# Kernel tuning notes

Measured on AMD Instinct MI355X. Metric: run time of the kernel, lower is better.

Reference implementation:

```python
import jax, jax.numpy as jnp
import numpy as np

NUM_HEAD = 16
HIDDEN = 1024
HEAD_DIM = HIDDEN // NUM_HEAD


def setup_inputs() -> dict:
    key = jax.random.key(0)
    k1, k2, k3, k4, k5 = jax.random.split(key, 5)
    scale = 0.02
    x = jax.random.normal(k1, (2, 2048, HIDDEN), dtype=jnp.float32)
    w_in = jax.random.normal(k2, (3 * HIDDEN, HIDDEN), dtype=jnp.float32) * scale
    b_in = jax.random.normal(k3, (3 * HIDDEN,), dtype=jnp.float32) * scale
    w_out = jax.random.normal(k4, (HIDDEN, HIDDEN), dtype=jnp.float32) * scale
    b_out = jax.random.normal(k5, (HIDDEN,), dtype=jnp.float32) * scale
    return {"x": x, "w_in": w_in, "b_in": b_in, "w_out": w_out, "b_out": b_out}


def reference(x, w_in, b_in, w_out, b_out):
    B, S, D = x.shape
    # in_proj: fused QKV, torch Linear convention y = x @ W.T + b
    qkv = x @ w_in.T + b_in                      # [B,S,3D]
    q, k, v = jnp.split(qkv, 3, axis=-1)         # each [B,S,D]
    def heads(t):
        return t.reshape(B, S, NUM_HEAD, HEAD_DIM).transpose(0, 2, 1, 3)  # [B,H,S,d]
    q, k, v = heads(q), heads(k), heads(v)
    scores = jnp.einsum("bhqd,bhkd->bhqk", q, k) / jnp.sqrt(
        jnp.asarray(HEAD_DIM, dtype=x.dtype))    # [B,H,S,S]
    attn = jax.nn.softmax(scores, axis=-1)
    out = jnp.einsum("bhqk,bhkd->bhqd", attn, v)  # [B,H,S,d]
    out = out.transpose(0, 2, 1, 3).reshape(B, S, D)
    return out @ w_out.T + b_out
```

## Files before the change

### kernel.cpp

```cpp
#include <hip/hip_runtime.h>

using u16 = unsigned short;
using u32 = unsigned int;

typedef __bf16 bf16x8 __attribute__((ext_vector_type(8)));
typedef __bf16 bf16x2 __attribute__((ext_vector_type(2)));
typedef float f32x4 __attribute__((ext_vector_type(4)));

__device__ __forceinline__ u16 f2b(float x) {
  u32 u = __builtin_bit_cast(u32, x);
  u += 0x7fffu + ((u >> 16) & 1u);
  return (u16)(u >> 16);
}

__device__ __forceinline__ u32 pk2(float lo, float hi) {
  bf16x2 t;
  t[0] = (__bf16)lo;
  t[1] = (__bf16)hi;
  return __builtin_bit_cast(u32, t);
}

__device__ __forceinline__ void gload16(const u16* g, u16* l) {
  __builtin_amdgcn_global_load_lds(
      (const __attribute__((address_space(1))) void*)g,
      (__attribute__((address_space(3))) void*)l, 16, 0, 0);
}

#define SCALE_Q 0.1803368801111204f
#define DEFER_THR 8.0f

__global__ void cvt_bf16_k(const float* __restrict__ s, u16* __restrict__ d, int n8) {
  int i = blockIdx.x * blockDim.x + threadIdx.x;
  int stride = gridDim.x * blockDim.x;
  for (; i < n8; i += stride) {
    float4 a = ((const float4*)s)[2 * i];
    float4 b = ((const float4*)s)[2 * i + 1];
    uint4 o;
    o.x = (u32)f2b(a.x) | ((u32)f2b(a.y) << 16);
    o.y = (u32)f2b(a.z) | ((u32)f2b(a.w) << 16);
    o.z = (u32)f2b(b.x) | ((u32)f2b(b.y) << 16);
    o.w = (u32)f2b(b.z) | ((u32)f2b(b.w) << 16);
    ((uint4*)d)[i] = o;
  }
}

template <int MODE, int BM>
__global__ __launch_bounds__(256) void gemm_bt(
    const u16* __restrict__ A, const u16* __restrict__ Bm,
    const float* __restrict__ bias,
    u16* __restrict__ q, u16* __restrict__ k, u16* __restrict__ v,
    float* __restrict__ outf) {
  constexpr int KD = 1024;
  constexpr int MR = BM / 32;
  constexpr int CA = BM / 8;
  const int n0 = blockIdx.x * 128;
  const int m0 = blockIdx.y * BM;
  const int tid = threadIdx.x;
  const int wid = tid >> 6;
  const int lane = tid & 63;
  const int wr = wid >> 1, wc = wid & 1;
  const int fr = lane & 15, fg = lane >> 4;
  const int srow = lane >> 3;
  const int scol = ((lane & 7) ^ (srow & 7)) * 8;

  __shared__ __align__(16) u16 As[BM * 64];
  __shared__ __align__(16) u16 Bs[128 * 64];

  f32x4 acc[MR][4] = {};

  for (int k0 = 0; k0 < KD; k0 += 64) {
#pragma unroll
    for (int i = 0; i < CA / 4; ++i) {
      const int chunk = wid * (CA / 4) + i;
      gload16(A + (size_t)(m0 + chunk * 8 + srow) * KD + k0 + scol, As + chunk * 512);
    }
#pragma unroll
    for (int i = 0; i < 4; ++i) {
      const int chunk = wid * 4 + i;
      gload16(Bm + (size_t)(n0 + chunk * 8 + srow) * KD + k0 + scol, Bs + chunk * 512);
    }
    __syncthreads();
#pragma unroll
    for (int ks = 0; ks < 2; ++ks) {
      bf16x8 af[MR], bfr[4];
#pragma unroll
      for (int r = 0; r < MR; ++r) {
        const int row = wr * (BM / 2) + r * 16 + fr;
        af[r] = *(const bf16x8*)(As + row * 64 + ((ks * 32 + fg * 8) ^ ((row & 7) * 8)));
      }
#pragma unroll
      for (int c = 0; c < 4; ++c) {
        const int row = wc * 64 + c * 16 + fr;
        bfr[c] = *(const bf16x8*)(Bs + row * 64 + ((ks * 32 + fg * 8) ^ ((row & 7) * 8)));
      }
#pragma unroll
      for (int r = 0; r < MR; ++r)
#pragma unroll
        for (int c = 0; c < 4; ++c)
          acc[r][c] = __builtin_amdgcn_mfma_f32_16x16x32_bf16(af[r], bfr[c], acc[r][c], 0, 0, 0);
    }
    __syncthreads();
  }

#pragma unroll
  for (int r = 0; r < MR; ++r) {
#pragma unroll
    for (int c = 0; c < 4; ++c) {
      const int gcol = n0 + wc * 64 + c * 16 + fr;
      const float bv = bias[gcol];
#pragma unroll
      for (int g = 0; g < 4; ++g) {
        const int grow = m0 + wr * (BM / 2) + r * 16 + fg * 4 + g;
        float val = acc[r][c][g] + bv;
        if (MODE == 0) {
          const int which = gcol >> 10;
          const int dcol = gcol & 1023;
          const int hh = dcol >> 6, dd = dcol & 63;
          const int bb = grow >> 11, ss = grow & 2047;
          const int bhk = (bb << 4) + hh;
          const int t = ss >> 6, sl = ss & 63;
          if (which == 0) {
            q[((size_t)bhk * 2048 + ss) * 64 + dd] = f2b(val * SCALE_Q);
          } else if (which == 1) {
            const int r_ = (sl & 32) | (((sl >> 2) & 1) << 4) | (((sl >> 4) & 1) << 3) |
                           (((sl >> 3) & 1) << 2) | (sl & 3);
            k[((size_t)bhk * 32 + t) * 4096 + r_ * 64 + (dd ^ ((r_ & 7) << 3))] = f2b(val);
          } else {
            v[((size_t)bhk * 32 + t) * 4096 + dd * 64 + (sl ^ ((dd & 7) << 3))] = f2b(val);
          }
        } else {
          outf[(size_t)grow * 1024 + gcol] = val;
        }
      }
    }
  }
}

__global__ __launch_bounds__(256) void attn_fwd(
    const u16* __restrict__ Q, const u16* __restrict__ KG,
    const u16* __restrict__ VG, u16* __restrict__ AO) {
  const int wg = blockIdx.x;
  const int newid = (wg & 7) * 64 + (wg >> 3);
  const int bh = newid >> 4;
  const int qt = newid & 15;
  const int b = bh >> 4, h = bh & 15;

  const int tid = threadIdx.x, wid = tid >> 6, lane = tid & 63;
  const int fr = lane & 15, fg = lane >> 4;
  const int q0 = qt * 128 + wid * 32;

  __shared__ __align__(16) u16 Ks[2][4096];
  __shared__ __align__(16) u16 Vs[2][4096];

  const size_t qbase = (size_t)bh * (2048 * 64);
  bf16x8 qf[2][2];
#pragma unroll
  for (int rf = 0; rf < 2; ++rf)
#pragma unroll
    for (int ks = 0; ks < 2; ++ks)
      qf[rf][ks] = *(const bf16x8*)(Q + qbase + (size_t)(q0 + rf * 16 + fr) * 64 + ks * 32 + fg * 8);

  f32x4 o[2][4] = {};
  float mrow[2] = {-3.0e38f, -3.0e38f};
  float lrow[2] = {0.f, 0.f};

  const u16* kg = KG + (size_t)bh * 131072 + tid * 8;
  const u16* vg = VG + (size_t)bh * 131072 + tid * 8;

#define STAGE(t, bufi) do {                                        \
    const u16* ksrc = kg + (t) * 4096;                             \
    const u16* vsrc = vg + (t) * 4096;                             \
    u16* kdst = (u16*)Ks[bufi] + wid * 512;                        \
    u16* vdst = (u16*)Vs[bufi] + wid * 512;                        \
    gload16(ksrc, kdst); gload16(ksrc + 2048, kdst + 2048);        \
    gload16(vsrc, vdst); gload16(vsrc + 2048, vdst + 2048);        \
  } while (0)

  STAGE(0, 0);
  __syncthreads();

  for (int t = 0; t < 32; ++t) {
    const int cur = t & 1;
    if (t + 1 < 32) STAGE(t + 1, cur ^ 1);
    const u16* kb = (const u16*)Ks[cur];
    const u16* vb = (const u16*)Vs[cur];

    bf16x8 kf[4][2], vf[4][2];
#pragma unroll
    for (int c = 0; c < 4; ++c)
#pragma unroll
      for (int ks = 0; ks < 2; ++ks)
        kf[c][ks] = *(const bf16x8*)(kb + (c * 16 + fr) * 64 + ((ks * 32 + fg * 8) ^ ((fr & 7) * 8)));
#pragma unroll
    for (int d = 0; d < 4; ++d)
#pragma unroll
      for (int ks = 0; ks < 2; ++ks)
        vf[d][ks] = *(const bf16x8*)(vb + (d * 16 + fr) * 64 + ((ks * 32 + fg * 8) ^ ((fr & 7) * 8)));

#pragma unroll
    for (int rf = 0; rf < 2; ++rf) {
      f32x4 p[4];
      __builtin_amdgcn_s_setprio(1);
#pragma unroll
      for (int c = 0; c < 4; ++c) {
        f32x4 z = {};
        z = __builtin_amdgcn_mfma_f32_16x16x32_bf16(kf[c][0], qf[rf][0], z, 0, 0, 0);
        z = __builtin_amdgcn_mfma_f32_16x16x32_bf16(kf[c][1], qf[rf][1], z, 0, 0, 0);
        p[c] = z;
      }
      __builtin_amdgcn_s_setprio(0);
      f32x4 m01 = __builtin_elementwise_max(p[0], p[1]);
      f32x4 m23 = __builtin_elementwise_max(p[2], p[3]);
      f32x4 m4 = __builtin_elementwise_max(m01, m23);
      float mx = fmaxf(fmaxf(m4[0], m4[1]), fmaxf(m4[2], m4[3]));
      mx = fmaxf(mx, __shfl_xor(mx, 16));
      mx = fmaxf(mx, __shfl_xor(mx, 32));

      const float mold = mrow[rf];
      const bool defer = __all(mx <= mold + DEFER_THR);
      float mnew = mold;
      if (!defer) {
        mnew = fmaxf(mold, mx);
        const float corr = __builtin_amdgcn_exp2f(mold - mnew);
        mrow[rf] = mnew;
        lrow[rf] *= corr;
#pragma unroll
        for (int d = 0; d < 4; ++d) o[rf][d] *= corr;
      }
#pragma unroll
      for (int c = 0; c < 4; ++c)
#pragma unroll
        for (int g = 0; g < 4; ++g)
          p[c][g] = __builtin_amdgcn_exp2f(p[c][g] - mnew);
      f32x4 s4 = (p[0] + p[1]) + (p[2] + p[3]);
      float rs = (s4[0] + s4[1]) + (s4[2] + s4[3]);
      rs += __shfl_xor(rs, 16);
      rs += __shfl_xor(rs, 32);
      lrow[rf] += rs;

      bf16x8 pa[2];
#pragma unroll
      for (int ks = 0; ks < 2; ++ks) {
        u32 w0 = pk2(p[2 * ks][0], p[2 * ks][1]);
        u32 w1 = pk2(p[2 * ks][2], p[2 * ks][3]);
        u32 w2 = pk2(p[2 * ks + 1][0], p[2 * ks + 1][1]);
        u32 w3 = pk2(p[2 * ks + 1][2], p[2 * ks + 1][3]);
        uint4 packed = {w0, w1, w2, w3};
        pa[ks] = __builtin_bit_cast(bf16x8, packed);
      }
      __builtin_amdgcn_s_setprio(1);
#pragma unroll
      for (int d = 0; d < 4; ++d) {
        o[rf][d] = __builtin_amdgcn_mfma_f32_16x16x32_bf16(vf[d][0], pa[0], o[rf][d], 0, 0, 0);
        o[rf][d] = __builtin_amdgcn_mfma_f32_16x16x32_bf16(vf[d][1], pa[1], o[rf][d], 0, 0, 0);
      }
      __builtin_amdgcn_s_setprio(0);
    }
    __syncthreads();
  }

#pragma unroll
  for (int rf = 0; rf < 2; ++rf) {
    const float rinv = __builtin_amdgcn_rcpf(lrow[rf]);
    const size_t rowoff = (size_t)(b * 2048 + q0 + rf * 16 + fr) * 1024 + h * 64;
#pragma unroll
    for (int d = 0; d < 4; ++d) {
      uint2 st;
      st.x = pk2(o[rf][d][0] * rinv, o[rf][d][1] * rinv);
      st.y = pk2(o[rf][d][2] * rinv, o[rf][d][3] * rinv);
      *(uint2*)(AO + rowoff + d * 16 + fg * 4) = st;
    }
  }
#undef STAGE
}

extern "C" void kernel_launch(void* const* d_in, const int* in_sizes, int n_in,
                              void* d_out, int out_size, void* d_ws, size_t ws_size,
                              hipStream_t stream) {
  (void)in_sizes; (void)n_in; (void)out_size; (void)ws_size;
  const float* x     = (const float*)d_in[0];
  const float* w_in  = (const float*)d_in[1];
  const float* b_in  = (const float*)d_in[2];
  const float* w_out = (const float*)d_in[3];
  const float* b_out = (const float*)d_in[4];

  u16* xb    = (u16*)d_ws;
  u16* winb  = xb    + (size_t)4096 * 1024;
  u16* woutb = winb  + (size_t)3072 * 1024;
  u16* qb    = woutb + (size_t)1024 * 1024;
  u16* kb    = qb    + (size_t)4194304;
  u16* vb    = kb    + (size_t)4194304;
  u16* aob   = vb    + (size_t)4194304;

  cvt_bf16_k<<<2048, 256, 0, stream>>>(x, xb, 4096 * 1024 / 8);
  cvt_bf16_k<<<1536, 256, 0, stream>>>(w_in, winb, 3072 * 1024 / 8);
  cvt_bf16_k<<<512, 256, 0, stream>>>(w_out, woutb, 1024 * 1024 / 8);

  gemm_bt<0, 128><<<dim3(24, 32), 256, 0, stream>>>(xb, winb, b_in, qb, kb, vb, nullptr);
  attn_fwd<<<512, 256, 0, stream>>>(qb, kb, vb, aob);
  gemm_bt<1, 64><<<dim3(8, 64), 256, 0, stream>>>(aob, woutb, b_out, nullptr, nullptr, nullptr,
                                                  (float*)d_out);
}
```

Baseline: 214.0 us.

## Merge conversions, vectorize V epilogue, prefetch two tiles, MFMA row sums

The three fp32-to-bf16 conversion launches become one kernel. The QKV GEMM epilogue now writes V as packed 8-byte stores instead of scalar stores. The attention kernel prefetches two K/V tiles ahead, using explicit vmcnt waits and barriers in place of __syncthreads. It also computes softmax row sums with an MFMA against a ones vector instead of shuffle reductions. These changes cut launch overhead, store instructions and cross-lane reductions, at the cost of delicate manual waitcnt and barrier placement. The last iterations also issue redundant wraparound loads.

```diff
diff --git a/kernel.cpp b/kernel.cpp
--- a/kernel.cpp
+++ b/kernel.cpp
@@ -29,19 +29,23 @@
 #define SCALE_Q 0.1803368801111204f
 #define DEFER_THR 8.0f
 
-__global__ void cvt_bf16_k(const float* __restrict__ s, u16* __restrict__ d, int n8) {
-  int i = blockIdx.x * blockDim.x + threadIdx.x;
-  int stride = gridDim.x * blockDim.x;
-  for (; i < n8; i += stride) {
-    float4 a = ((const float4*)s)[2 * i];
-    float4 b = ((const float4*)s)[2 * i + 1];
-    uint4 o;
-    o.x = (u32)f2b(a.x) | ((u32)f2b(a.y) << 16);
-    o.y = (u32)f2b(a.z) | ((u32)f2b(a.w) << 16);
-    o.z = (u32)f2b(b.x) | ((u32)f2b(b.y) << 16);
-    o.w = (u32)f2b(b.z) | ((u32)f2b(b.w) << 16);
-    ((uint4*)d)[i] = o;
-  }
+__global__ __launch_bounds__(256) void cvt_all_k(
+    const float* __restrict__ x, const float* __restrict__ w_in,
+    const float* __restrict__ w_out, u16* __restrict__ dst) {
+  const int i = blockIdx.x * 256 + threadIdx.x;
+  const float* s;
+  int j;
+  if (i < 524288) { s = x; j = i; }
+  else if (i < 917504) { s = w_in; j = i - 524288; }
+  else { s = w_out; j = i - 917504; }
+  float4 a = ((const float4*)s)[2 * j];
+  float4 b = ((const float4*)s)[2 * j + 1];
+  uint4 o;
+  o.x = (u32)f2b(a.x) | ((u32)f2b(a.y) << 16);
+  o.y = (u32)f2b(a.z) | ((u32)f2b(a.w) << 16);
+  o.z = (u32)f2b(b.x) | ((u32)f2b(b.y) << 16);
+  o.w = (u32)f2b(b.z) | ((u32)f2b(b.w) << 16);
+  ((uint4*)dst)[i] = o;
 }
 
 template <int MODE, int BM>
@@ -108,28 +112,38 @@
     for (int c = 0; c < 4; ++c) {
       const int gcol = n0 + wc * 64 + c * 16 + fr;
       const float bv = bias[gcol];
-#pragma unroll
-      for (int g = 0; g < 4; ++g) {
-        const int grow = m0 + wr * (BM / 2) + r * 16 + fg * 4 + g;
-        float val = acc[r][c][g] + bv;
-        if (MODE == 0) {
-          const int which = gcol >> 10;
-          const int dcol = gcol & 1023;
-          const int hh = dcol >> 6, dd = dcol & 63;
-          const int bb = grow >> 11, ss = grow & 2047;
-          const int bhk = (bb << 4) + hh;
-          const int t = ss >> 6, sl = ss & 63;
-          if (which == 0) {
-            q[((size_t)bhk * 2048 + ss) * 64 + dd] = f2b(val * SCALE_Q);
-          } else if (which == 1) {
+      if (MODE == 0) {
+        const int which = gcol >> 10;
+        const int dcol = gcol & 1023;
+        const int hh = dcol >> 6, dd = dcol & 63;
+        const int grow0 = m0 + wr * (BM / 2) + r * 16 + fg * 4;
+        const int bb = grow0 >> 11, ss0 = grow0 & 2047;
+        const int bhk = (bb << 4) + hh;
+        const int t = ss0 >> 6, sl0 = ss0 & 63;
+        if (which == 2) {
+          uint2 st;
+          st.x = pk2(acc[r][c][0] + bv, acc[r][c][1] + bv);
+          st.y = pk2(acc[r][c][2] + bv, acc[r][c][3] + bv);
+          *(uint2*)(v + ((size_t)bhk * 32 + t) * 4096 + dd * 64 + (sl0 ^ ((dd & 7) << 3))) = st;
+        } else if (which == 1) {
+#pragma unroll
+          for (int g = 0; g < 4; ++g) {
+            const int sl = sl0 + g;
             const int r_ = (sl & 32) | (((sl >> 2) & 1) << 4) | (((sl >> 4) & 1) << 3) |
                            (((sl >> 3) & 1) << 2) | (sl & 3);
-            k[((size_t)bhk * 32 + t) * 4096 + r_ * 64 + (dd ^ ((r_ & 7) << 3))] = f2b(val);
-          } else {
-            v[((size_t)bhk * 32 + t) * 4096 + dd * 64 + (sl ^ ((dd & 7) << 3))] = f2b(val);
+            k[((size_t)bhk * 32 + t) * 4096 + r_ * 64 + (dd ^ ((r_ & 7) << 3))] =
+                f2b(acc[r][c][g] + bv);
           }
         } else {
-          outf[(size_t)grow * 1024 + gcol] = val;
+#pragma unroll
+          for (int g = 0; g < 4; ++g)
+            q[((size_t)bhk * 2048 + ss0 + g) * 64 + dd] = f2b((acc[r][c][g] + bv) * SCALE_Q);
+        }
+      } else {
+#pragma unroll
+        for (int g = 0; g < 4; ++g) {
+          const int grow = m0 + wr * (BM / 2) + r * 16 + fg * 4 + g;
+          outf[(size_t)grow * 1024 + gcol] = acc[r][c][g] + bv;
         }
       }
     }
@@ -160,9 +174,13 @@
     for (int ks = 0; ks < 2; ++ks)
       qf[rf][ks] = *(const bf16x8*)(Q + qbase + (size_t)(q0 + rf * 16 + fr) * 64 + ks * 32 + fg * 8);
 
+  bf16x8 onef;
+#pragma unroll
+  for (int i = 0; i < 8; ++i) onef[i] = (__bf16)1.0f;
+
   f32x4 o[2][4] = {};
+  f32x4 l4[2] = {};
   float mrow[2] = {-3.0e38f, -3.0e38f};
-  float lrow[2] = {0.f, 0.f};
 
   const u16* kg = KG + (size_t)bh * 131072 + tid * 8;
   const u16* vg = VG + (size_t)bh * 131072 + tid * 8;
@@ -177,14 +195,15 @@
   } while (0)
 
   STAGE(0, 0);
-  __syncthreads();
+  STAGE(1, 1);
 
   for (int t = 0; t < 32; ++t) {
     const int cur = t & 1;
-    if (t + 1 < 32) STAGE(t + 1, cur ^ 1);
+    asm volatile("s_waitcnt vmcnt(4)" ::: "memory");
+    __builtin_amdgcn_s_barrier();
+
     const u16* kb = (const u16*)Ks[cur];
     const u16* vb = (const u16*)Vs[cur];
-
     bf16x8 kf[4][2], vf[4][2];
 #pragma unroll
     for (int c = 0; c < 4; ++c)
@@ -196,6 +215,10 @@
 #pragma unroll
       for (int ks = 0; ks < 2; ++ks)
         vf[d][ks] = *(const bf16x8*)(vb + (d * 16 + fr) * 64 + ((ks * 32 + fg * 8) ^ ((fr & 7) * 8)));
+    asm volatile("s_waitcnt lgkmcnt(0)" ::: "memory");
+    __builtin_amdgcn_sched_barrier(0);
+    __builtin_amdgcn_s_barrier();
+    STAGE((t + 2) & 31, cur);
 
 #pragma unroll
     for (int rf = 0; rf < 2; ++rf) {
@@ -223,7 +246,7 @@
         mnew = fmaxf(mold, mx);
         const float corr = __builtin_amdgcn_exp2f(mold - mnew);
         mrow[rf] = mnew;
-        lrow[rf] *= corr;
+        l4[rf] *= corr;
 #pragma unroll
         for (int d = 0; d < 4; ++d) o[rf][d] *= corr;
       }
@@ -232,11 +255,6 @@
 #pragma unroll
         for (int g = 0; g < 4; ++g)
           p[c][g] = __builtin_amdgcn_exp2f(p[c][g] - mnew);
-      f32x4 s4 = (p[0] + p[1]) + (p[2] + p[3]);
-      float rs = (s4[0] + s4[1]) + (s4[2] + s4[3]);
-      rs += __shfl_xor(rs, 16);
-      rs += __shfl_xor(rs, 32);
-      lrow[rf] += rs;
 
       bf16x8 pa[2];
 #pragma unroll
@@ -249,6 +267,8 @@
         pa[ks] = __builtin_bit_cast(bf16x8, packed);
       }
       __builtin_amdgcn_s_setprio(1);
+      l4[rf] = __builtin_amdgcn_mfma_f32_16x16x32_bf16(onef, pa[0], l4[rf], 0, 0, 0);
+      l4[rf] = __builtin_amdgcn_mfma_f32_16x16x32_bf16(onef, pa[1], l4[rf], 0, 0, 0);
 #pragma unroll
       for (int d = 0; d < 4; ++d) {
         o[rf][d] = __builtin_amdgcn_mfma_f32_16x16x32_bf16(vf[d][0], pa[0], o[rf][d], 0, 0, 0);
@@ -256,12 +276,12 @@
       }
       __builtin_amdgcn_s_setprio(0);
     }
-    __syncthreads();
   }
+  asm volatile("s_waitcnt vmcnt(0)" ::: "memory");
 
 #pragma unroll
   for (int rf = 0; rf < 2; ++rf) {
-    const float rinv = __builtin_amdgcn_rcpf(lrow[rf]);
+    const float rinv = __builtin_amdgcn_rcpf(l4[rf][0]);
     const size_t rowoff = (size_t)(b * 2048 + q0 + rf * 16 + fr) * 1024 + h * 64;
 #pragma unroll
     for (int d = 0; d < 4; ++d) {
@@ -292,9 +312,7 @@
   u16* vb    = kb    + (size_t)4194304;
   u16* aob   = vb    + (size_t)4194304;
 
-  cvt_bf16_k<<<2048, 256, 0, stream>>>(x, xb, 4096 * 1024 / 8);
-  cvt_bf16_k<<<1536, 256, 0, stream>>>(w_in, winb, 3072 * 1024 / 8);
-  cvt_bf16_k<<<512, 256, 0, stream>>>(w_out, woutb, 1024 * 1024 / 8);
+  cvt_all_k<<<4096, 256, 0, stream>>>(x, w_in, w_out, xb);
 
   gemm_bt<0, 128><<<dim3(24, 32), 256, 0, stream>>>(xb, winb, b_in, qb, kb, vb, nullptr);
   attn_fwd<<<512, 256, 0, stream>>>(qb, kb, vb, aob);
```

New measurement: 198.7 us. -7.2%, faster.
